# Optimization experiments

Measured on AMD Instinct MI355X. Metric: run time of the kernel, lower is better.

The kernel has to match this reference:

```python
import jax, jax.numpy as jnp
import numpy as np

B, S, H, NH = 2, 1024, 1024, 16
SE, E = 512, 1024
NEXP, TOPK, FF = 8, 2, 2048
HD = H // NH
EPS = 1e-6
THETA = 10000.0
NEG = -1e9


def _rms(x, w):
    return x * jax.lax.rsqrt(jnp.mean(x * x, axis=-1, keepdims=True) + EPS) * w


def _rope(q, k, pos):
    # q,k: [B,S,NH,HD]; pos: [B,S] int
    inv = 1.0 / (THETA ** (jnp.arange(0, HD, 2, dtype=jnp.float32) / HD))
    f = pos[..., None].astype(jnp.float32) * inv            # [B,S,HD/2]
    emb = jnp.concatenate([f, f], axis=-1)                  # [B,S,HD]
    cos = jnp.cos(emb)[:, :, None, :]
    sin = jnp.sin(emb)[:, :, None, :]
    def rot(x):
        x1, x2 = jnp.split(x, 2, axis=-1)
        return jnp.concatenate([-x2, x1], axis=-1)
    return q * cos + rot(q) * sin, k * cos + rot(k) * sin


def _forward(hidden_states, encoder_hidden_states,
             in_ln_w, wq, wk, wv, wo,
             c_norm_w, cq_w, cq_b, ck_w, ck_b, cv_w, cv_b, co_w, co_b,
             post_ln_w, gate_w, w1, w2, w3,
             position_ids, encoder_attention_mask):
    x = hidden_states

    # ---- self-attention (RMSNorm pre-norm, RoPE, causal) ----
    res = x
    h = _rms(x, in_ln_w)
    q = (h @ wq.T).reshape(B, S, NH, HD)
    k = (h @ wk.T).reshape(B, S, NH, HD)
    v = (h @ wv.T).reshape(B, S, NH, HD)
    q, k = _rope(q, k, position_ids)
    scores = jnp.einsum('bqhd,bkhd->bhqk', q, k) / np.sqrt(HD)
    causal = jnp.tril(jnp.ones((S, S), dtype=bool))
    scores = jnp.where(causal, scores, NEG)
    attn = jax.nn.softmax(scores, axis=-1)
    o = jnp.einsum('bhqk,bkhd->bqhd', attn, v).reshape(B, S, H) @ wo.T
    x = res + o

    # ---- cross-attention block (RMSNorm, MHA with kdim=vdim=E, bias) ----
    res = x
    h = _rms(x, c_norm_w)
    cq = (h @ cq_w.T + cq_b).reshape(B, S, NH, HD)
    ck = (encoder_hidden_states @ ck_w.T + ck_b).reshape(B, SE, NH, HD)
    cv = (encoder_hidden_states @ cv_w.T + cv_b).reshape(B, SE, NH, HD)
    sc = jnp.einsum('bqhd,bkhd->bhqk', cq, ck) / np.sqrt(HD)
    pad = (encoder_attention_mask == 0)                     # key_padding_mask
    sc = jnp.where(pad[:, None, None, :], NEG, sc)
    ca = jax.nn.softmax(sc, axis=-1)
    o = jnp.einsum('bhqk,bkhd->bqhd', ca, cv).reshape(B, S, H) @ co_w.T + co_b
    x = res + o

    # ---- block-sparse MoE FFN (top-2 routing, SwiGLU experts) ----
    res = x
    h = _rms(x, post_ln_w).reshape(-1, H)                   # [T,H], T=B*S
    logits = h @ gate_w.T                                    # [T,NEXP]
    probs = jax.nn.softmax(logits, axis=-1)
    topv, topi = jax.lax.top_k(probs, TOPK)                  # [T,TOPK]
    topv = topv / jnp.sum(topv, axis=-1, keepdims=True)
    out = jnp.zeros_like(h)
    for e in range(NEXP):  # fixed small expert loop
        we = jnp.sum(jnp.where(topi == e, topv, 0.0), axis=-1)   # [T]
        ff = (jax.nn.silu(h @ w1[e].T) * (h @ w3[e].T)) @ w2[e].T
        out = out + we[:, None] * ff
    x = res + out.reshape(B, S, H)
    return x


def setup_inputs() -> dict:
    key = jax.random.key(0)
    ks = jax.random.split(key, 24)
    sc = 0.02
    d = {
        'hidden_states': jax.random.normal(ks[0], (B, S, H), jnp.float32),
        'position_ids': jnp.broadcast_to(jnp.arange(S, dtype=jnp.int64), (B, S)),
        'encoder_hidden_states': jax.random.normal(ks[1], (B, SE, E), jnp.float32),
        'encoder_attention_mask': jnp.ones((B, SE), jnp.int64),
        'in_ln_w': jnp.ones((H,), jnp.float32),
        'wq': jax.random.normal(ks[2], (H, H), jnp.float32) * sc,
        'wk': jax.random.normal(ks[3], (H, H), jnp.float32) * sc,
        'wv': jax.random.normal(ks[4], (H, H), jnp.float32) * sc,
        'wo': jax.random.normal(ks[5], (H, H), jnp.float32) * sc,
        'c_norm_w': jnp.ones((H,), jnp.float32),
        'cq_w': jax.random.normal(ks[6], (H, H), jnp.float32) * sc,
        'cq_b': jnp.zeros((H,), jnp.float32),
        'ck_w': jax.random.normal(ks[7], (H, E), jnp.float32) * sc,
        'ck_b': jnp.zeros((H,), jnp.float32),
        'cv_w': jax.random.normal(ks[8], (H, E), jnp.float32) * sc,
        'cv_b': jnp.zeros((H,), jnp.float32),
        'co_w': jax.random.normal(ks[9], (H, H), jnp.float32) * sc,
        'co_b': jnp.zeros((H,), jnp.float32),
        'post_ln_w': jnp.ones((H,), jnp.float32),
        'gate_w': jax.random.normal(ks[10], (NEXP, H), jnp.float32) * sc,
        'w1': jax.random.normal(ks[11], (NEXP, FF, H), jnp.float32) * sc,
        'w2': jax.random.normal(ks[12], (NEXP, H, FF), jnp.float32) * sc,
        'w3': jax.random.normal(ks[13], (NEXP, FF, H), jnp.float32) * sc,
    }
    return d


def reference(hidden_states, position_ids, encoder_hidden_states, encoder_attention_mask,
              in_ln_w, wq, wk, wv, wo,
              c_norm_w, cq_w, cq_b, ck_w, ck_b, cv_w, cv_b, co_w, co_b,
              post_ln_w, gate_w, w1, w2, w3):
    return _forward(hidden_states, encoder_hidden_states,
                    in_ln_w, wq, wk, wv, wo,
                    c_norm_w, cq_w, cq_b, ck_w, ck_b, cv_w, cv_b, co_w, co_b,
                    post_ln_w, gate_w, w1, w2, w3,
                    position_ids, encoder_attention_mask)
```

## Files before the change

kernel.cpp:

```cpp
#include <hip/hip_runtime.h>

#define B_    2
#define S_    1024
#define H_    1024
#define NH_   16
#define HD_   64
#define SE_   512
#define E_    1024
#define NEXP_ 8
#define FF_   2048
#define T_    (B_*S_)
#define TE_   (B_*SE_)
#define PERM_MAX 6400
#define MAXRT 24

typedef short v8s __attribute__((ext_vector_type(8)));
typedef short v4s __attribute__((ext_vector_type(4)));
typedef float v4f __attribute__((ext_vector_type(4)));
typedef _Float16 v8h __attribute__((ext_vector_type(8)));
typedef _Float16 v4h __attribute__((ext_vector_type(4)));

__device__ __forceinline__ unsigned short f2b(float f) {
  unsigned int u = __float_as_uint(f);
  u = (u + 0x7FFFu + ((u >> 16) & 1u)) >> 16;
  return (unsigned short)u;
}

__device__ __forceinline__ void g2l16(const void* g, void* l) {
  __builtin_amdgcn_global_load_lds(
      (const __attribute__((address_space(1))) unsigned int*)g,
      (__attribute__((address_space(3))) unsigned int*)l, 16, 0, 0);
}

__global__ void detect_kern(const int* __restrict__ pos, const int* __restrict__ msk,
                            int* __restrict__ flags, int* __restrict__ counts) {
  if (threadIdx.x < 16) counts[threadIdx.x] = 0;
  if (threadIdx.x == 0) {
    flags[0] = (pos[1] == 1) ? 0 : 1;
    flags[1] = (msk[1] == 1) ? 0 : 1;
  }
}

struct SplitArgs {
  const float* src[9];
  _Float16* dh[9];
  _Float16* dl[9];
};
__global__ __launch_bounds__(256)
void split_all(SplitArgs sa) {
  int b = blockIdx.x;
  int seg, i;
  if (b < 4096) { seg = b >> 9; i = (b & 511) * 256 + threadIdx.x; }
  else          { seg = 8;      i = (b - 4096) * 256 + threadIdx.x; }
  const float* x = sa.src[seg];
  v4f a = *(const v4f*)&x[i * 8];
  v4f c = *(const v4f*)&x[i * 8 + 4];
  v8h hv, lv;
  #pragma unroll
  for (int j = 0; j < 8; ++j) {
    float v = j < 4 ? a[j] : c[j - 4];
    _Float16 hh = (_Float16)v;
    hv[j] = hh; lv[j] = (_Float16)(v - (float)hh);
  }
  *(v8h*)&sa.dh[seg][i * 8] = hv;
  *(v8h*)&sa.dl[seg][i * 8] = lv;
}

__global__ __launch_bounds__(256)
void cvt_all(const float* __restrict__ s0, const float* __restrict__ s1,
             const float* __restrict__ s2,
             unsigned short* __restrict__ d0, unsigned short* __restrict__ d1,
             unsigned short* __restrict__ d2) {
  int b = blockIdx.x;
  int seg = b >> 14;
  int i = (b & 16383) * 256 + threadIdx.x;
  const float* x = seg == 0 ? s0 : (seg == 1 ? s1 : s2);
  unsigned short* y = seg == 0 ? d0 : (seg == 1 ? d1 : d2);
  v4f v = *(const v4f*)&x[i * 4];
  v4s o;
  #pragma unroll
  for (int j = 0; j < 4; ++j) o[j] = (short)f2b(v[j]);
  *(v4s*)&y[i * 4] = o;
}

__global__ __launch_bounds__(256)
void rmsnorm_hl_kern(const float* __restrict__ x, const float* __restrict__ w,
                     _Float16* __restrict__ yh, _Float16* __restrict__ yl) {
  int row = blockIdx.x, tid = threadIdx.x;
  const float* xr = x + (long)row * 1024;
  v4f v = *(const v4f*)&xr[tid * 4];
  float ss = v[0]*v[0] + v[1]*v[1] + v[2]*v[2] + v[3]*v[3];
  #pragma unroll
  for (int off = 32; off; off >>= 1) ss += __shfl_xor(ss, off);
  __shared__ float sw[4];
  if ((tid & 63) == 0) sw[tid >> 6] = ss;
  __syncthreads();
  float tot = sw[0] + sw[1] + sw[2] + sw[3];
  float rs = rsqrtf(tot * (1.0f / 1024.0f) + 1e-6f);
  const float* wr = w + tid * 4;
  v4h oh, ol;
  #pragma unroll
  for (int j = 0; j < 4; ++j) {
    float f = v[j] * rs * wr[j];
    _Float16 hh = (_Float16)f;
    oh[j] = hh; ol[j] = (_Float16)(f - (float)hh);
  }
  *(v4h*)&yh[(long)row * 1024 + tid * 4] = oh;
  *(v4h*)&yl[(long)row * 1024 + tid * 4] = ol;
}

__global__ __launch_bounds__(256)
void rmsnorm_kern(const float* __restrict__ x, const float* __restrict__ w,
                  unsigned short* __restrict__ y) {
  int row = blockIdx.x, tid = threadIdx.x;
  const float* xr = x + (long)row * 1024;
  v4f v = *(const v4f*)&xr[tid * 4];
  float ss = v[0]*v[0] + v[1]*v[1] + v[2]*v[2] + v[3]*v[3];
  #pragma unroll
  for (int off = 32; off; off >>= 1) ss += __shfl_xor(ss, off);
  __shared__ float sw[4];
  if ((tid & 63) == 0) sw[tid >> 6] = ss;
  __syncthreads();
  float tot = sw[0] + sw[1] + sw[2] + sw[3];
  float rs = rsqrtf(tot * (1.0f / 1024.0f) + 1e-6f);
  const float* wr = w + tid * 4;
  v4s o;
  #pragma unroll
  for (int j = 0; j < 4; ++j) o[j] = (short)f2b(v[j] * rs * wr[j]);
  *(v4s*)&y[(long)row * 1024 + tid * 4] = o;
}

__global__ __launch_bounds__(256)
void rope_split_kern(float* __restrict__ q, const float* __restrict__ k,
                     _Float16* __restrict__ kh, _Float16* __restrict__ kl,
                     const int* __restrict__ pos, const int* __restrict__ flags) {
  int g = blockIdx.x * 256 + threadIdx.x;
  int d = g & 31;
  int h = (g >> 5) & 15;
  int s = (g >> 9) & (S_ - 1);
  int b = g >> 19;
  long base = (((long)(b * S_ + s)) * NH_ + h) * HD_;
  int pidx = b * S_ + s;
  int pv = pos[flags[0] ? (pidx << 1) : pidx];
  float p = (float)pv;
  float inv = powf(10000.0f, -(float)d * (1.0f / 32.0f));
  float f = p * inv;
  float sn = sinf(f), cs = cosf(f);
  float q1 = q[base + d], q2 = q[base + d + 32];
  q[base + d]      = q1 * cs - q2 * sn;
  q[base + d + 32] = q2 * cs + q1 * sn;
  float k1 = k[base + d], k2 = k[base + d + 32];
  float kr1 = k1 * cs - k2 * sn;
  float kr2 = k2 * cs + k1 * sn;
  _Float16 hh = (_Float16)kr1;
  kh[base + d] = hh; kl[base + d] = (_Float16)(kr1 - (float)hh);
  hh = (_Float16)kr2;
  kh[base + d + 32] = hh; kl[base + d + 32] = (_Float16)(kr2 - (float)hh);
}

__global__ __launch_bounds__(256)
void vtrans_kern(const float* __restrict__ vf, _Float16* __restrict__ vth,
                 _Float16* __restrict__ vtl, int Sk) {
  int kb = blockIdx.x, bh = blockIdx.y;
  int b = bh >> 4, h = bh & 15;
  int t = threadIdx.x;
  __shared__ float tile[64][65];
  int key = t >> 2, dsub = (t & 3) * 16;
  const float* src = vf + (((long)(b * Sk + kb * 64 + key)) * NH_ + h) * HD_ + dsub;
  #pragma unroll
  for (int j = 0; j < 16; j += 4) *(v4f*)&tile[key][dsub + j] = *(const v4f*)&src[j];
  __syncthreads();
  int d = t >> 2, ksub = (t & 3) * 16;
  v8h hv0, lv0, hv1, lv1;
  #pragma unroll
  for (int j = 0; j < 16; ++j) {
    float v = tile[ksub + j][d];
    _Float16 hh = (_Float16)v;
    if (j < 8) { hv0[j] = hh; lv0[j] = (_Float16)(v - (float)hh); }
    else       { hv1[j - 8] = hh; lv1[j - 8] = (_Float16)(v - (float)hh); }
  }
  long ob = (((long)(b * NH_ + h)) * HD_ + d) * Sk + kb * 64 + ksub;
  *(v8h*)&vth[ob] = hv0; *(v8h*)&vth[ob + 8] = hv1;
  *(v8h*)&vtl[ob] = lv0; *(v8h*)&vtl[ob + 8] = lv1;
}

struct ZArg {
  const _Float16 *Ah, *Al, *Bh, *Bl;
  const float *bias, *resid;
  float *Cf;
  float *Cf2;
  _Float16 *Ch, *Cl;
  int M;
};

__global__ __launch_bounds__(256)
void gemm_hl(ZArg z0, ZArg z1, ZArg z2, int K) {
  ZArg za = blockIdx.z == 0 ? z0 : (blockIdx.z == 1 ? z1 : z2);
  int flat = blockIdx.x;
  int wg = (flat & 7) * 32 + (flat >> 3);
  int row0 = (wg >> 4) * 128;
  int col0 = (wg & 15) * 64;
  if (row0 >= za.M) return;
  int tid = threadIdx.x, lane = tid & 63, w = tid >> 6;
  int lr = lane & 15, lg = lane >> 4;
  int wr = w >> 1, wc = w & 1;
  int rsw = (lr >> 1) & 3;

  __shared__ _Float16 Ah_s[2][128 * 32], Al_s[2][128 * 32];
  __shared__ _Float16 Bh_s[2][64 * 32], Bl_s[2][64 * 32];

  int av0 = w * 64 + lane, av1 = (w + 4) * 64 + lane;
  int ar0 = av0 >> 2, as0 = (av0 & 3) ^ ((ar0 >> 1) & 3);
  int ar1 = av1 >> 2, as1 = (av1 & 3) ^ ((ar1 >> 1) & 3);
  int bv = w * 64 + lane;
  int br = bv >> 2, bs = (bv & 3) ^ ((br >> 1) & 3);
  const _Float16* ga0h = za.Ah + (long)(row0 + ar0) * K + as0 * 8;
  const _Float16* ga0l = za.Al + (long)(row0 + ar0) * K + as0 * 8;
  const _Float16* ga1h = za.Ah + (long)(row0 + ar1) * K + as1 * 8;
  const _Float16* ga1l = za.Al + (long)(row0 + ar1) * K + as1 * 8;
  const _Float16* gbh  = za.Bh + (long)(col0 + br) * K + bs * 8;
  const _Float16* gbl  = za.Bl + (long)(col0 + br) * K + bs * 8;

  auto stage = [&](int buf, int k0) {
    g2l16(ga0h + k0, (char*)Ah_s[buf] + w * 1024);
    g2l16(ga1h + k0, (char*)Ah_s[buf] + (w + 4) * 1024);
    g2l16(ga0l + k0, (char*)Al_s[buf] + w * 1024);
    g2l16(ga1l + k0, (char*)Al_s[buf] + (w + 4) * 1024);
    g2l16(gbh + k0, (char*)Bh_s[buf] + w * 1024);
    g2l16(gbl + k0, (char*)Bl_s[buf] + w * 1024);
  };

  v4f acc[4][2] = {};
  stage(0, 0);
  int cur = 0;

  for (int k0 = 0; k0 < K; k0 += 32) {
    __syncthreads();
    if (k0 + 32 < K) stage(cur ^ 1, k0 + 32);

    v8h ah[4], al[4], bh[2], bl[2];
    #pragma unroll
    for (int m = 0; m < 4; ++m) {
      int off = (wr * 64 + m * 16 + lr) * 64 + ((lg ^ rsw) << 4);
      ah[m] = *(const v8h*)((char*)Ah_s[cur] + off);
      al[m] = *(const v8h*)((char*)Al_s[cur] + off);
    }
    #pragma unroll
    for (int n = 0; n < 2; ++n) {
      int off = (wc * 32 + n * 16 + lr) * 64 + ((lg ^ rsw) << 4);
      bh[n] = *(const v8h*)((char*)Bh_s[cur] + off);
      bl[n] = *(const v8h*)((char*)Bl_s[cur] + off);
    }
    #pragma unroll
    for (int m = 0; m < 4; ++m)
      #pragma unroll
      for (int n = 0; n < 2; ++n) {
        acc[m][n] = __builtin_amdgcn_mfma_f32_16x16x32_f16(ah[m], bh[n], acc[m][n], 0, 0, 0);
        acc[m][n] = __builtin_amdgcn_mfma_f32_16x16x32_f16(ah[m], bl[n], acc[m][n], 0, 0, 0);
        acc[m][n] = __builtin_amdgcn_mfma_f32_16x16x32_f16(al[m], bh[n], acc[m][n], 0, 0, 0);
      }
    cur ^= 1;
  }

  #pragma unroll
  for (int m = 0; m < 4; ++m) {
    int rbase = row0 + wr * 64 + m * 16 + lg * 4;
    #pragma unroll
    for (int n = 0; n < 2; ++n) {
      int gcol = col0 + wc * 32 + n * 16 + lr;
      float bb = za.bias ? za.bias[gcol] : 0.0f;
      #pragma unroll
      for (int rr = 0; rr < 4; ++rr) {
        long idx = (long)(rbase + rr) * 1024 + gcol;
        float v = acc[m][n][rr] + bb;
        if (za.Cf) {
          float r = za.resid ? (za.resid[idx] + v) : v;
          za.Cf[idx] = r;
          if (za.Cf2) za.Cf2[idx] = r;
        } else {
          _Float16 hh = (_Float16)v;
          za.Ch[idx] = hh;
          za.Cl[idx] = (_Float16)(v - (float)hh);
        }
      }
    }
  }
}

template<bool CAUSAL>
__global__ __launch_bounds__(256)
void attn_hl(const float* __restrict__ Q,
             const _Float16* __restrict__ Khg, const _Float16* __restrict__ Klg,
             const _Float16* __restrict__ Vhg, const _Float16* __restrict__ Vlg,
             _Float16* __restrict__ Oh, _Float16* __restrict__ Ol,
             const int* __restrict__ mask, const int* __restrict__ flags,
             int Sq, int Sk, float qscale) {
  int flat = blockIdx.x;
  int wgA = (flat & 7) * 64 + (flat >> 3);
  int qt = wgA & 15, bh = wgA >> 4;
  int b = bh >> 4, h = bh & 15;
  int tid = threadIdx.x, lane = tid & 63, w = tid >> 6;
  int lr = lane & 15, lg = lane >> 4;
  int q0 = qt * 64;
  int mf = (!CAUSAL && mask) ? flags[1] : 0;
  int swz = lr & 7;

  __shared__ _Float16 Kh_s[64 * 64], Kl_s[64 * 64];
  __shared__ _Float16 Vh_s[64 * 64], Vl_s[64 * 64];
  __shared__ _Float16 Psh[4][16][72], Psl[4][16][72];

  v8h qh[2], ql[2];
  {
    long qbase = ((long)(b * Sq + q0 + w * 16 + lr) * NH_ + h) * HD_;
    #pragma unroll
    for (int kk = 0; kk < 2; ++kk) {
      v4f f0 = *(const v4f*)&Q[qbase + kk * 32 + lg * 8];
      v4f f1 = *(const v4f*)&Q[qbase + kk * 32 + lg * 8 + 4];
      #pragma unroll
      for (int j = 0; j < 8; ++j) {
        float f = (j < 4 ? f0[j] : f1[j - 4]) * qscale;
        _Float16 hh = (_Float16)f;
        qh[kk][j] = hh;
        ql[kk][j] = (_Float16)(f - (float)hh);
      }
    }
  }
  v4f of[4] = {};
  float m4[4], l4[4];
  #pragma unroll
  for (int i = 0; i < 4; ++i) { m4[i] = -3e38f; l4[i] = 0.0f; }

  int nkt = CAUSAL ? (qt + 1) : (Sk >> 6);
  for (int kt = 0; kt < nkt; ++kt) {
    __syncthreads();
    #pragma unroll
    for (int i = 0; i < 2; ++i) {
      int c = w + i * 4;
      int v = c * 64 + lane;
      int row = v >> 3, c8 = v & 7;
      int sc = (c8 ^ (row & 7)) << 3;
      long kb = ((long)(b * Sk + kt * 64 + row) * NH_ + h) * HD_ + sc;
      g2l16(Khg + kb, (char*)Kh_s + c * 1024);
      g2l16(Klg + kb, (char*)Kl_s + c * 1024);
      long vb = ((long)(b * NH_ + h) * HD_ + row) * Sk + kt * 64 + sc;
      g2l16(Vhg + vb, (char*)Vh_s + c * 1024);
      g2l16(Vlg + vb, (char*)Vl_s + c * 1024);
    }
    __syncthreads();

    v4f sf[4] = {};
    #pragma unroll
    for (int kk = 0; kk < 2; ++kk)
      #pragma unroll
      for (int n = 0; n < 4; ++n) {
        int off = (n * 16 + lr) * 128 + ((((kk << 2) | lg) ^ swz) << 4);
        v8h kbh = *(const v8h*)((char*)Kh_s + off);
        v8h kbl = *(const v8h*)((char*)Kl_s + off);
        sf[n] = __builtin_amdgcn_mfma_f32_16x16x32_f16(qh[kk], kbh, sf[n], 0, 0, 0);
        sf[n] = __builtin_amdgcn_mfma_f32_16x16x32_f16(qh[kk], kbl, sf[n], 0, 0, 0);
        sf[n] = __builtin_amdgcn_mfma_f32_16x16x32_f16(ql[kk], kbh, sf[n], 0, 0, 0);
      }

    if constexpr (CAUSAL) {
      if (kt == qt) {
        #pragma unroll
        for (int n = 0; n < 4; ++n) {
          int kcol = kt * 64 + n * 16 + lr;
          #pragma unroll
          for (int rr = 0; rr < 4; ++rr) {
            int qr = q0 + w * 16 + lg * 4 + rr;
            if (kcol > qr) sf[n][rr] = -1e9f;
          }
        }
      }
    } else {
      if (mask) {
        #pragma unroll
        for (int n = 0; n < 4; ++n) {
          int kcol = kt * 64 + n * 16 + lr;
          int mi = b * Sk + kcol;
          if (mask[mf ? (mi << 1) : mi] == 0) {
            #pragma unroll
            for (int rr = 0; rr < 4; ++rr) sf[n][rr] = -1e9f;
          }
        }
      }
    }

    float al[4];
    #pragma unroll
    for (int rr = 0; rr < 4; ++rr) {
      float mx = fmaxf(fmaxf(sf[0][rr], sf[1][rr]), fmaxf(sf[2][rr], sf[3][rr]));
      #pragma unroll
      for (int off = 8; off; off >>= 1) mx = fmaxf(mx, __shfl_xor(mx, off));
      float mn = fmaxf(m4[rr], mx);
      al[rr] = __expf(m4[rr] - mn);
      m4[rr] = mn;
      float rs = 0.0f;
      #pragma unroll
      for (int n = 0; n < 4; ++n) {
        float pv = __expf(sf[n][rr] - mn);
        sf[n][rr] = pv;
        rs += pv;
      }
      #pragma unroll
      for (int off = 8; off; off >>= 1) rs += __shfl_xor(rs, off);
      l4[rr] = l4[rr] * al[rr] + rs;
    }

    #pragma unroll
    for (int n = 0; n < 4; ++n)
      #pragma unroll
      for (int rr = 0; rr < 4; ++rr) {
        of[n][rr] *= al[rr];
        float pv = sf[n][rr];
        _Float16 ph = (_Float16)pv;
        Psh[w][lg * 4 + rr][n * 16 + lr] = ph;
        Psl[w][lg * 4 + rr][n * 16 + lr] = (_Float16)(pv - (float)ph);
      }
    __syncthreads();

    #pragma unroll
    for (int kc = 0; kc < 2; ++kc) {
      v8h pah = *(const v8h*)&Psh[w][lr][kc * 32 + lg * 8];
      v8h pal = *(const v8h*)&Psl[w][lr][kc * 32 + lg * 8];
      #pragma unroll
      for (int n = 0; n < 4; ++n) {
        int off = (n * 16 + lr) * 128 + ((((kc << 2) | lg) ^ swz) << 4);
        v8h vbh = *(const v8h*)((char*)Vh_s + off);
        v8h vbl = *(const v8h*)((char*)Vl_s + off);
        of[n] = __builtin_amdgcn_mfma_f32_16x16x32_f16(pah, vbh, of[n], 0, 0, 0);
        of[n] = __builtin_amdgcn_mfma_f32_16x16x32_f16(pah, vbl, of[n], 0, 0, 0);
        of[n] = __builtin_amdgcn_mfma_f32_16x16x32_f16(pal, vbh, of[n], 0, 0, 0);
      }
    }
  }

  #pragma unroll
  for (int rr = 0; rr < 4; ++rr) {
    int qr = q0 + w * 16 + lg * 4 + rr;
    float inv = 1.0f / l4[rr];
    long ob = (long)(b * Sq + qr) * 1024 + h * 64;
    #pragma unroll
    for (int n = 0; n < 4; ++n) {
      float v = of[n][rr] * inv;
      _Float16 hh = (_Float16)v;
      Oh[ob + n * 16 + lr] = hh;
      Ol[ob + n * 16 + lr] = (_Float16)(v - (float)hh);
    }
  }
}

__global__ __launch_bounds__(512)
void moe_gemm1(const unsigned short* __restrict__ A,
               const unsigned short* __restrict__ B1,
               const unsigned short* __restrict__ B2,
               unsigned short* __restrict__ Cb,
               const int* __restrict__ tm_e, const int* __restrict__ tm_slot,
               const int* __restrict__ ntl, const int* __restrict__ perm) {
  int flat = blockIdx.x;
  int wg = (flat & 7) * 96 + (flat >> 3);
  int tile = wg >> 5;
  if (tile >= ntl[0]) return;
  int col0 = (wg & 31) * 64;
  int e = tm_e[tile];
  int row0 = tm_slot[tile];
  const unsigned short* Bp1 = B1 + (long)e * (FF_ * H_);
  const unsigned short* Bp2 = B2 + (long)e * (FF_ * H_);
  int tid = threadIdx.x, lane = tid & 63, w = tid >> 6;
  int lr = lane & 15, lg = lane >> 4;
  int wr = w >> 1, wc = w & 1;
  int rsw = (lr >> 1) & 3;

  __shared__ unsigned short As[2][256 * 32];
  __shared__ unsigned short Bs1[2][64 * 32];
  __shared__ unsigned short Bs2[2][64 * 32];

  const unsigned short* ga[2];
  #pragma unroll
  for (int i = 0; i < 2; ++i) {
    int c = i * 512 + tid;
    int r = c >> 2, sub = (c & 3) ^ ((r >> 1) & 3);
    int tok = perm[row0 + r];
    ga[i] = A + (long)(tok < 0 ? 0 : tok) * H_ + sub * 8;
  }
  int bc = tid & 255;
  int rb = bc >> 2, sb = (bc & 3) ^ ((rb >> 1) & 3);
  const unsigned short* gB = (tid < 256 ? Bp1 : Bp2) + (long)(col0 + rb) * H_ + sb * 8;
  size_t lBoff = (size_t)((w & 3) * 64) * 8;

  auto stage = [&](int buf, int k0) {
    #pragma unroll
    for (int i = 0; i < 2; ++i)
      g2l16(ga[i] + k0, As[buf] + (size_t)(i * 512 + w * 64) * 8);
    g2l16(gB + k0, (tid < 256 ? Bs1[buf] : Bs2[buf]) + lBoff);
  };

  v4f acc[4][2] = {};
  v4f acc2[4][2] = {};
  stage(0, 0);
  int cur = 0;

  for (int k0 = 0; k0 < H_; k0 += 32) {
    __syncthreads();
    if (k0 + 32 < H_) stage(cur ^ 1, k0 + 32);

    v8s a[4], b1[2], b2[2];
    #pragma unroll
    for (int m = 0; m < 4; ++m)
      a[m] = *(const v8s*)&As[cur][(wr * 64 + m * 16 + lr) * 32 + (lg ^ rsw) * 8];
    #pragma unroll
    for (int n = 0; n < 2; ++n) {
      b1[n] = *(const v8s*)&Bs1[cur][(wc * 32 + n * 16 + lr) * 32 + (lg ^ rsw) * 8];
      b2[n] = *(const v8s*)&Bs2[cur][(wc * 32 + n * 16 + lr) * 32 + (lg ^ rsw) * 8];
    }
    #pragma unroll
    for (int m = 0; m < 4; ++m)
      #pragma unroll
      for (int n = 0; n < 2; ++n) {
        acc[m][n]  = __builtin_amdgcn_mfma_f32_16x16x32_bf16(a[m], b1[n], acc[m][n], 0, 0, 0);
        acc2[m][n] = __builtin_amdgcn_mfma_f32_16x16x32_bf16(a[m], b2[n], acc2[m][n], 0, 0, 0);
      }
    cur ^= 1;
  }

  #pragma unroll
  for (int m = 0; m < 4; ++m) {
    int grow = row0 + wr * 64 + m * 16 + lg * 4;
    #pragma unroll
    for (int n = 0; n < 2; ++n) {
      int gcol = col0 + wc * 32 + n * 16 + lr;
      #pragma unroll
      for (int rr = 0; rr < 4; ++rr) {
        float v = acc[m][n][rr];
        float g = v / (1.0f + __expf(-v));
        Cb[(long)(grow + rr) * FF_ + gcol] = f2b(g * acc2[m][n][rr]);
      }
    }
  }
}

__global__ __launch_bounds__(256)
void moe_gemm2(const unsigned short* __restrict__ A,
               const unsigned short* __restrict__ B,
               float* __restrict__ Cf,
               const int* __restrict__ tm_e, const int* __restrict__ tm_slot,
               const int* __restrict__ ntl,
               const int* __restrict__ perm, const float* __restrict__ pwgt) {
  int flat = blockIdx.x;
  int wg = (flat & 7) * 96 + (flat >> 3);
  int t2 = wg >> 4;
  int tile = t2 >> 1;
  if (tile >= ntl[0]) return;
  int row0 = tm_slot[tile] + (t2 & 1) * 128;
  int col0 = (wg & 15) * 64;
  int e = tm_e[tile];
  const unsigned short* Bp = B + (long)e * (H_ * FF_);
  int tid = threadIdx.x, lane = tid & 63, w = tid >> 6;
  int lr = lane & 15, lg = lane >> 4;
  int rsw = (lr >> 1) & 3;

  __shared__ unsigned short As[2][128 * 32];
  __shared__ unsigned short Bs[2][64 * 32];

  const unsigned short* ga[2];
  #pragma unroll
  for (int i = 0; i < 2; ++i) {
    int c = i * 256 + tid;
    int r = c >> 2, sub = (c & 3) ^ ((r >> 1) & 3);
    ga[i] = A + (long)(row0 + r) * FF_ + sub * 8;
  }
  int rb = tid >> 2, sb = (tid & 3) ^ ((rb >> 1) & 3);
  const unsigned short* gb = Bp + (long)(col0 + rb) * FF_ + sb * 8;

  auto stage = [&](int buf, int k0) {
    #pragma unroll
    for (int i = 0; i < 2; ++i)
      g2l16(ga[i] + k0, As[buf] + (size_t)(i * 256 + w * 64) * 8);
    g2l16(gb + k0, Bs[buf] + (size_t)(w * 64) * 8);
  };

  v4f acc[2][4] = {};
  stage(0, 0);
  int cur = 0;

  for (int k0 = 0; k0 < FF_; k0 += 32) {
    __syncthreads();
    if (k0 + 32 < FF_) stage(cur ^ 1, k0 + 32);

    v8s a[2], b[4];
    #pragma unroll
    for (int m = 0; m < 2; ++m)
      a[m] = *(const v8s*)&As[cur][(w * 32 + m * 16 + lr) * 32 + (lg ^ rsw) * 8];
    #pragma unroll
    for (int n = 0; n < 4; ++n)
      b[n] = *(const v8s*)&Bs[cur][(n * 16 + lr) * 32 + (lg ^ rsw) * 8];
    #pragma unroll
    for (int m = 0; m < 2; ++m)
      #pragma unroll
      for (int n = 0; n < 4; ++n)
        acc[m][n] = __builtin_amdgcn_mfma_f32_16x16x32_bf16(a[m], b[n], acc[m][n], 0, 0, 0);
    cur ^= 1;
  }

  #pragma unroll
  for (int m = 0; m < 2; ++m) {
    int grow = row0 + w * 32 + m * 16 + lg * 4;
    #pragma unroll
    for (int rr = 0; rr < 4; ++rr) {
      int tok = perm[grow + rr];
      if (tok < 0) continue;
      float pw = pwgt[grow + rr];
      #pragma unroll
      for (int n = 0; n < 4; ++n) {
        int gcol = col0 + n * 16 + lr;
        atomicAdd(&Cf[(long)tok * H_ + gcol], acc[m][n][rr] * pw);
      }
    }
  }
}

__global__ __launch_bounds__(64)
void router_kern(const float* __restrict__ x, const float* __restrict__ w,
                 const float* __restrict__ gw,
                 int* __restrict__ topi, float* __restrict__ topw,
                 int* __restrict__ counts) {
  int t = blockIdx.x, lane = threadIdx.x;
  const float* xr = x + (long)t * 1024;
  float vals[16];
  float ss = 0.0f;
  #pragma unroll
  for (int i = 0; i < 16; ++i) { float v = xr[lane + i * 64]; vals[i] = v; ss += v * v; }
  #pragma unroll
  for (int off = 32; off; off >>= 1) ss += __shfl_xor(ss, off);
  float rs = rsqrtf(ss * (1.0f / 1024.0f) + 1e-6f);
  #pragma unroll
  for (int i = 0; i < 16; ++i) vals[i] *= rs * w[lane + i * 64];
  float lgts[8];
  #pragma unroll
  for (int e = 0; e < 8; ++e) {
    const float* g = gw + e * 1024;
    float s = 0.0f;
    #pragma unroll
    for (int i = 0; i < 16; ++i) s += vals[i] * g[lane + i * 64];
    #pragma unroll
    for (int off = 32; off; off >>= 1) s += __shfl_xor(s, off);
    lgts[e] = s;
  }
  int i1 = 0; float l1 = lgts[0];
  #pragma unroll
  for (int e = 1; e < 8; ++e) if (lgts[e] > l1) { l1 = lgts[e]; i1 = e; }
  int i2 = -1; float l2 = -3e38f;
  #pragma unroll
  for (int e = 0; e < 8; ++e) if (e != i1 && lgts[e] > l2) { l2 = lgts[e]; i2 = e; }
  float w1 = 1.0f / (1.0f + __expf(l2 - l1));
  if (lane == 0) {
    topi[t * 2] = i1; topi[t * 2 + 1] = i2;
    topw[t * 2] = w1; topw[t * 2 + 1] = 1.0f - w1;
    atomicAdd(&counts[i1], 1);
    atomicAdd(&counts[i2], 1);
  }
}

__global__ __launch_bounds__(256)
void route_pack_kern(const int* __restrict__ counts,
                     const int* __restrict__ topi, const float* __restrict__ topw,
                     int* __restrict__ poff,
                     int* __restrict__ tm_e, int* __restrict__ tm_slot,
                     int* __restrict__ ntl,
                     int* __restrict__ perm, float* __restrict__ pwgt) {
  __shared__ int s_poff[8];
  __shared__ int s_cur[8];
  __shared__ int stot;
  if (threadIdx.x < 8) s_cur[threadIdx.x] = 0;
  if (threadIdx.x == 0) {
    int off = 0, nt = 0;
    for (int e = 0; e < 8; ++e) {
      s_poff[e] = off; poff[e] = off;
      int c = counts[e];
      int ntE = (c + 255) >> 8;
      for (int i = 0; i < ntE; ++i) { tm_e[nt] = e; tm_slot[nt] = off + i * 256; ++nt; }
      off += ntE * 256;
    }
    ntl[0] = nt; ntl[1] = off;
    stot = off;
  }
  __syncthreads();
  for (int s = threadIdx.x; s < stot; s += 256) perm[s] = -1;
  __syncthreads();
  for (int t = threadIdx.x; t < T_; t += 256) {
    #pragma unroll
    for (int kk = 0; kk < 2; ++kk) {
      int e = topi[t * 2 + kk];
      int pos = atomicAdd(&s_cur[e], 1);
      int slot = s_poff[e] + pos;
      perm[slot] = t;
      pwgt[slot] = topw[t * 2 + kk];
    }
  }
}

extern "C" void kernel_launch(void* const* d_in, const int* in_sizes, int n_in,
                              void* d_out, int out_size, void* d_ws, size_t ws_size,
                              hipStream_t stream) {
  (void)in_sizes; (void)n_in; (void)out_size; (void)ws_size;
  const float* x_in  = (const float*)d_in[0];
  const int*  posids = (const int*)d_in[1];
  const float* enc   = (const float*)d_in[2];
  const int*  emask  = (const int*)d_in[3];
  const float* inln  = (const float*)d_in[4];
  const float* wq    = (const float*)d_in[5];
  const float* wk    = (const float*)d_in[6];
  const float* wv    = (const float*)d_in[7];
  const float* wo    = (const float*)d_in[8];
  const float* cnorm = (const float*)d_in[9];
  const float* cqw   = (const float*)d_in[10];
  const float* cqb   = (const float*)d_in[11];
  const float* ckw   = (const float*)d_in[12];
  const float* ckb   = (const float*)d_in[13];
  const float* cvw   = (const float*)d_in[14];
  const float* cvb   = (const float*)d_in[15];
  const float* cow   = (const float*)d_in[16];
  const float* cob   = (const float*)d_in[17];
  const float* pln   = (const float*)d_in[18];
  const float* gatew = (const float*)d_in[19];
  const float* w1    = (const float*)d_in[20];
  const float* w2    = (const float*)d_in[21];
  const float* w3    = (const float*)d_in[22];
  float* out = (float*)d_out;

  char* p = (char*)d_ws;
  auto alloc = [&](size_t bytes) -> char* {
    char* r = p;
    p += (bytes + 255) & ~(size_t)255;
    return r;
  };
  const size_t MB = 1024 * 1024;
  char* A1 = alloc(4 * MB);
  char* A2 = alloc(4 * MB);
  char* Bq = alloc(8 * MB);
  char* Bk = alloc(8 * MB);
  char* Bv = alloc(8 * MB);
  char* C1 = alloc(4 * MB);
  char* C2 = alloc(4 * MB);
  char* D1 = alloc(4 * MB);
  char* D2 = alloc(4 * MB);
  float* x1 = (float*)alloc(8 * MB);
  float* x2 = (float*)alloc(8 * MB);
  unsigned short* h3b = (unsigned short*)alloc(4 * MB);
  _Float16* ench = (_Float16*)alloc(2 * MB);
  _Float16* encl = (_Float16*)alloc(2 * MB);
  int*   meta    = (int*)alloc(4 * (8 + 8 + 8 + 2 + 2 + MAXRT + MAXRT));
  int*   counts  = meta;
  int*   poff    = meta + 16;
  int*   ntl     = meta + 24;
  int*   flags   = meta + 26;
  int*   tm_e    = meta + 28;
  int*   tm_slot = meta + 28 + MAXRT;
  int*   topi    = (int*)alloc((size_t)T_ * 2 * 4);
  float* topw    = (float*)alloc((size_t)T_ * 2 * 4);
  int*   perm    = (int*)alloc((size_t)PERM_MAX * 4);
  float* pwgt    = (float*)alloc((size_t)PERM_MAX * 4);
  unsigned short* w1b = (unsigned short*)alloc((size_t)NEXP_ * FF_ * H_ * 2);
  unsigned short* w3b = (unsigned short*)alloc((size_t)NEXP_ * FF_ * H_ * 2);
  unsigned short* w2b = (unsigned short*)alloc((size_t)NEXP_ * H_ * FF_ * 2);

  _Float16 *hh = (_Float16*)A1, *hl = (_Float16*)A2;
  _Float16 *oh = (_Float16*)A1, *ol = (_Float16*)A2;
  _Float16 *ckh = (_Float16*)A1, *ckl = (_Float16*)A2;
  float* qf = (float*)Bq;  float* cqf = (float*)Bq;
  float* kf = (float*)Bk;
  _Float16 *cvth = (_Float16*)Bk, *cvtl = (_Float16*)(Bk + 4 * MB);
  float* vf = (float*)Bv;  float* cvf = (float*)Bv;
  _Float16 *kh = (_Float16*)C1, *kl = (_Float16*)C2;
  _Float16 *h2h = (_Float16*)C1, *h2l = (_Float16*)C2;
  _Float16 *vth = (_Float16*)D1, *vtl = (_Float16*)D2;
  _Float16 *coh = (_Float16*)D1, *col = (_Float16*)D2;
  unsigned short* ffh = (unsigned short*)Bq;
  _Float16* wsp = (_Float16*)w1b;
  auto wsph = [&](int i) { return wsp + (size_t)i * 2097152; };
  auto wspl = [&](int i) { return wsp + (size_t)i * 2097152 + 1048576; };

  dim3 blk(256);

  detect_kern<<<1, 64, 0, stream>>>(posids, emask, flags, counts);

  {
    SplitArgs sa;
    const float* wlist[8] = {wq, wk, wv, wo, cqw, ckw, cvw, cow};
    for (int i = 0; i < 8; ++i) { sa.src[i] = wlist[i]; sa.dh[i] = wsph(i); sa.dl[i] = wspl(i); }
    sa.src[8] = enc; sa.dh[8] = ench; sa.dl[8] = encl;
    split_all<<<4608, blk, 0, stream>>>(sa);
  }

  rmsnorm_hl_kern<<<T_, blk, 0, stream>>>(x_in, inln, hh, hl);
  {
    ZArg zq = {hh, hl, wsph(0), wspl(0), nullptr, nullptr, qf, nullptr, nullptr, nullptr, 2048};
    ZArg zk = {hh, hl, wsph(1), wspl(1), nullptr, nullptr, kf, nullptr, nullptr, nullptr, 2048};
    ZArg zv = {hh, hl, wsph(2), wspl(2), nullptr, nullptr, vf, nullptr, nullptr, nullptr, 2048};
    gemm_hl<<<dim3(256, 1, 3), blk, 0, stream>>>(zq, zk, zv, 1024);
  }
  rope_split_kern<<<(B_ * S_ * NH_ * 32) / 256, blk, 0, stream>>>(qf, kf, kh, kl, posids, flags);
  vtrans_kern<<<dim3(16, 32), blk, 0, stream>>>(vf, vth, vtl, 1024);
  attn_hl<true><<<512, blk, 0, stream>>>(
      qf, kh, kl, vth, vtl, oh, ol, nullptr, flags, 1024, 1024, 0.125f);
  {
    ZArg zo = {oh, ol, wsph(3), wspl(3), nullptr, x_in, x1, nullptr, nullptr, nullptr, 2048};
    gemm_hl<<<dim3(256, 1, 1), blk, 0, stream>>>(zo, zo, zo, 1024);
  }

  rmsnorm_hl_kern<<<T_, blk, 0, stream>>>(x1, cnorm, h2h, h2l);
  {
    ZArg zcq = {h2h, h2l, wsph(4), wspl(4), cqb, nullptr, cqf, nullptr, nullptr, nullptr, 2048};
    ZArg zck = {ench, encl, wsph(5), wspl(5), ckb, nullptr, nullptr, nullptr, ckh, ckl, 1024};
    ZArg zcv = {ench, encl, wsph(6), wspl(6), cvb, nullptr, cvf, nullptr, nullptr, nullptr, 1024};
    gemm_hl<<<dim3(256, 1, 3), blk, 0, stream>>>(zcq, zck, zcv, 1024);
  }
  vtrans_kern<<<dim3(8, 32), blk, 0, stream>>>(cvf, cvth, cvtl, 512);
  attn_hl<false><<<512, blk, 0, stream>>>(
      cqf, ckh, ckl, cvth, cvtl, coh, col, emask, flags, 1024, 512, 0.125f);
  {
    ZArg zco = {coh, col, wsph(7), wspl(7), cob, x1, x2, out, nullptr, nullptr, 2048};
    gemm_hl<<<dim3(256, 1, 1), blk, 0, stream>>>(zco, zco, zco, 1024);
  }

  cvt_all<<<49152, blk, 0, stream>>>(w1, w3, w2, w1b, w3b, w2b);
  rmsnorm_kern<<<T_, blk, 0, stream>>>(x2, pln, h3b);
  router_kern<<<T_, dim3(64), 0, stream>>>(x2, pln, gatew, topi, topw, counts);
  route_pack_kern<<<1, blk, 0, stream>>>(counts, topi, topw, poff, tm_e, tm_slot,
                                         ntl, perm, pwgt);
  moe_gemm1<<<768, dim3(512), 0, stream>>>(
      h3b, w1b, w3b, ffh, tm_e, tm_slot, ntl, perm);
  moe_gemm2<<<768, blk, 0, stream>>>(
      ffh, w2b, out, tm_e, tm_slot, ntl, perm, pwgt);
}
```

Measured before the change: 539.1 us.

## Fuse expert weight fp32-to-bf16 conversion into MoE GEMM staging loads

```diff
diff --git a/kernel.cpp b/kernel.cpp
--- a/kernel.cpp
+++ b/kernel.cpp
@@ -64,23 +64,6 @@
   }
   *(v8h*)&sa.dh[seg][i * 8] = hv;
   *(v8h*)&sa.dl[seg][i * 8] = lv;
-}
-
-__global__ __launch_bounds__(256)
-void cvt_all(const float* __restrict__ s0, const float* __restrict__ s1,
-             const float* __restrict__ s2,
-             unsigned short* __restrict__ d0, unsigned short* __restrict__ d1,
-             unsigned short* __restrict__ d2) {
-  int b = blockIdx.x;
-  int seg = b >> 14;
-  int i = (b & 16383) * 256 + threadIdx.x;
-  const float* x = seg == 0 ? s0 : (seg == 1 ? s1 : s2);
-  unsigned short* y = seg == 0 ? d0 : (seg == 1 ? d1 : d2);
-  v4f v = *(const v4f*)&x[i * 4];
-  v4s o;
-  #pragma unroll
-  for (int j = 0; j < 4; ++j) o[j] = (short)f2b(v[j]);
-  *(v4s*)&y[i * 4] = o;
 }
 
 __global__ __launch_bounds__(256)
@@ -453,8 +436,8 @@
 
 __global__ __launch_bounds__(512)
 void moe_gemm1(const unsigned short* __restrict__ A,
-               const unsigned short* __restrict__ B1,
-               const unsigned short* __restrict__ B2,
+               const float* __restrict__ B1,
+               const float* __restrict__ B2,
                unsigned short* __restrict__ Cb,
                const int* __restrict__ tm_e, const int* __restrict__ tm_slot,
                const int* __restrict__ ntl, const int* __restrict__ perm) {
@@ -465,8 +448,8 @@
   int col0 = (wg & 31) * 64;
   int e = tm_e[tile];
   int row0 = tm_slot[tile];
-  const unsigned short* Bp1 = B1 + (long)e * (FF_ * H_);
-  const unsigned short* Bp2 = B2 + (long)e * (FF_ * H_);
+  const float* Bp1 = B1 + (long)e * (FF_ * H_);
+  const float* Bp2 = B2 + (long)e * (FF_ * H_);
   int tid = threadIdx.x, lane = tid & 63, w = tid >> 6;
   int lr = lane & 15, lg = lane >> 4;
   int wr = w >> 1, wc = w & 1;
@@ -486,14 +469,19 @@
   }
   int bc = tid & 255;
   int rb = bc >> 2, sb = (bc & 3) ^ ((rb >> 1) & 3);
-  const unsigned short* gB = (tid < 256 ? Bp1 : Bp2) + (long)(col0 + rb) * H_ + sb * 8;
-  size_t lBoff = (size_t)((w & 3) * 64) * 8;
+  const float* gB = (tid < 256 ? Bp1 : Bp2) + (long)(col0 + rb) * H_ + sb * 8;
+  int lBoff = bc * 8;
 
   auto stage = [&](int buf, int k0) {
+    v4f b0 = *(const v4f*)&gB[k0];
+    v4f b1 = *(const v4f*)&gB[k0 + 4];
     #pragma unroll
     for (int i = 0; i < 2; ++i)
       g2l16(ga[i] + k0, As[buf] + (size_t)(i * 512 + w * 64) * 8);
-    g2l16(gB + k0, (tid < 256 ? Bs1[buf] : Bs2[buf]) + lBoff);
+    v8s hv;
+    #pragma unroll
+    for (int j = 0; j < 8; ++j) hv[j] = (short)f2b(j < 4 ? b0[j] : b1[j - 4]);
+    *(v8s*)&((tid < 256 ? Bs1 : Bs2)[buf][lBoff]) = hv;
   };
 
   v4f acc[4][2] = {};
@@ -505,21 +493,21 @@
     __syncthreads();
     if (k0 + 32 < H_) stage(cur ^ 1, k0 + 32);
 
-    v8s a[4], b1[2], b2[2];
+    v8s a[4], b1v[2], b2v[2];
     #pragma unroll
     for (int m = 0; m < 4; ++m)
       a[m] = *(const v8s*)&As[cur][(wr * 64 + m * 16 + lr) * 32 + (lg ^ rsw) * 8];
     #pragma unroll
     for (int n = 0; n < 2; ++n) {
-      b1[n] = *(const v8s*)&Bs1[cur][(wc * 32 + n * 16 + lr) * 32 + (lg ^ rsw) * 8];
-      b2[n] = *(const v8s*)&Bs2[cur][(wc * 32 + n * 16 + lr) * 32 + (lg ^ rsw) * 8];
+      b1v[n] = *(const v8s*)&Bs1[cur][(wc * 32 + n * 16 + lr) * 32 + (lg ^ rsw) * 8];
+      b2v[n] = *(const v8s*)&Bs2[cur][(wc * 32 + n * 16 + lr) * 32 + (lg ^ rsw) * 8];
     }
     #pragma unroll
     for (int m = 0; m < 4; ++m)
       #pragma unroll
       for (int n = 0; n < 2; ++n) {
-        acc[m][n]  = __builtin_amdgcn_mfma_f32_16x16x32_bf16(a[m], b1[n], acc[m][n], 0, 0, 0);
-        acc2[m][n] = __builtin_amdgcn_mfma_f32_16x16x32_bf16(a[m], b2[n], acc2[m][n], 0, 0, 0);
+        acc[m][n]  = __builtin_amdgcn_mfma_f32_16x16x32_bf16(a[m], b1v[n], acc[m][n], 0, 0, 0);
+        acc2[m][n] = __builtin_amdgcn_mfma_f32_16x16x32_bf16(a[m], b2v[n], acc2[m][n], 0, 0, 0);
       }
     cur ^= 1;
   }
@@ -542,7 +530,7 @@
 
 __global__ __launch_bounds__(256)
 void moe_gemm2(const unsigned short* __restrict__ A,
-               const unsigned short* __restrict__ B,
+               const float* __restrict__ B,
                float* __restrict__ Cf,
                const int* __restrict__ tm_e, const int* __restrict__ tm_slot,
                const int* __restrict__ ntl,
@@ -555,7 +543,7 @@
   int row0 = tm_slot[tile] + (t2 & 1) * 128;
   int col0 = (wg & 15) * 64;
   int e = tm_e[tile];
-  const unsigned short* Bp = B + (long)e * (H_ * FF_);
+  const float* Bp = B + (long)e * (H_ * FF_);
   int tid = threadIdx.x, lane = tid & 63, w = tid >> 6;
   int lr = lane & 15, lg = lane >> 4;
   int rsw = (lr >> 1) & 3;
@@ -571,13 +559,19 @@
     ga[i] = A + (long)(row0 + r) * FF_ + sub * 8;
   }
   int rb = tid >> 2, sb = (tid & 3) ^ ((rb >> 1) & 3);
-  const unsigned short* gb = Bp + (long)(col0 + rb) * FF_ + sb * 8;
+  const float* gb = Bp + (long)(col0 + rb) * FF_ + sb * 8;
+  int lBoff = tid * 8;
 
   auto stage = [&](int buf, int k0) {
+    v4f b0 = *(const v4f*)&gb[k0];
+    v4f b1 = *(const v4f*)&gb[k0 + 4];
     #pragma unroll
     for (int i = 0; i < 2; ++i)
       g2l16(ga[i] + k0, As[buf] + (size_t)(i * 256 + w * 64) * 8);
-    g2l16(gb + k0, Bs[buf] + (size_t)(w * 64) * 8);
+    v8s hv;
+    #pragma unroll
+    for (int j = 0; j < 8; ++j) hv[j] = (short)f2b(j < 4 ? b0[j] : b1[j - 4]);
+    *(v8s*)&Bs[buf][lBoff] = hv;
   };
 
   v4f acc[2][4] = {};
@@ -761,9 +755,7 @@
   float* topw    = (float*)alloc((size_t)T_ * 2 * 4);
   int*   perm    = (int*)alloc((size_t)PERM_MAX * 4);
   float* pwgt    = (float*)alloc((size_t)PERM_MAX * 4);
-  unsigned short* w1b = (unsigned short*)alloc((size_t)NEXP_ * FF_ * H_ * 2);
-  unsigned short* w3b = (unsigned short*)alloc((size_t)NEXP_ * FF_ * H_ * 2);
-  unsigned short* w2b = (unsigned short*)alloc((size_t)NEXP_ * H_ * FF_ * 2);
+  _Float16* wsp  = (_Float16*)alloc(32 * MB);
 
   _Float16 *hh = (_Float16*)A1, *hl = (_Float16*)A2;
   _Float16 *oh = (_Float16*)A1, *ol = (_Float16*)A2;
@@ -777,7 +769,6 @@
   _Float16 *vth = (_Float16*)D1, *vtl = (_Float16*)D2;
   _Float16 *coh = (_Float16*)D1, *col = (_Float16*)D2;
   unsigned short* ffh = (unsigned short*)Bq;
-  _Float16* wsp = (_Float16*)w1b;
   auto wsph = [&](int i) { return wsp + (size_t)i * 2097152; };
   auto wspl = [&](int i) { return wsp + (size_t)i * 2097152 + 1048576; };
 
@@ -824,13 +815,12 @@
     gemm_hl<<<dim3(256, 1, 1), blk, 0, stream>>>(zco, zco, zco, 1024);
   }
 
-  cvt_all<<<49152, blk, 0, stream>>>(w1, w3, w2, w1b, w3b, w2b);
   rmsnorm_kern<<<T_, blk, 0, stream>>>(x2, pln, h3b);
   router_kern<<<T_, dim3(64), 0, stream>>>(x2, pln, gatew, topi, topw, counts);
   route_pack_kern<<<1, blk, 0, stream>>>(counts, topi, topw, poff, tm_e, tm_slot,
                                          ntl, perm, pwgt);
   moe_gemm1<<<768, dim3(512), 0, stream>>>(
-      h3b, w1b, w3b, ffh, tm_e, tm_slot, ntl, perm);
+      h3b, w1, w3, ffh, tm_e, tm_slot, ntl, perm);
   moe_gemm2<<<768, blk, 0, stream>>>(
-      ffh, w2b, out, tm_e, tm_slot, ntl, perm, pwgt);
-}
+      ffh, w2, out, tm_e, tm_slot, ntl, perm, pwgt);
+}
```

Result: slower. 550.8 us (+2.2%).

## Fold MoE weight bf16 conversion into attention GEMMs and RMSNorm kernels

Applied to the files above, without the earlier changes.

```diff
diff --git a/kernel.cpp b/kernel.cpp
--- a/kernel.cpp
+++ b/kernel.cpp
@@ -67,23 +67,6 @@
 }
 
 __global__ __launch_bounds__(256)
-void cvt_all(const float* __restrict__ s0, const float* __restrict__ s1,
-             const float* __restrict__ s2,
-             unsigned short* __restrict__ d0, unsigned short* __restrict__ d1,
-             unsigned short* __restrict__ d2) {
-  int b = blockIdx.x;
-  int seg = b >> 14;
-  int i = (b & 16383) * 256 + threadIdx.x;
-  const float* x = seg == 0 ? s0 : (seg == 1 ? s1 : s2);
-  unsigned short* y = seg == 0 ? d0 : (seg == 1 ? d1 : d2);
-  v4f v = *(const v4f*)&x[i * 4];
-  v4s o;
-  #pragma unroll
-  for (int j = 0; j < 4; ++j) o[j] = (short)f2b(v[j]);
-  *(v4s*)&y[i * 4] = o;
-}
-
-__global__ __launch_bounds__(256)
 void rmsnorm_hl_kern(const float* __restrict__ x, const float* __restrict__ w,
                      _Float16* __restrict__ yh, _Float16* __restrict__ yl) {
   int row = blockIdx.x, tid = threadIdx.x;
@@ -111,7 +94,8 @@
 
 __global__ __launch_bounds__(256)
 void rmsnorm_kern(const float* __restrict__ x, const float* __restrict__ w,
-                  unsigned short* __restrict__ y) {
+                  unsigned short* __restrict__ y,
+                  const float* __restrict__ csrc, unsigned short* __restrict__ cdst) {
   int row = blockIdx.x, tid = threadIdx.x;
   const float* xr = x + (long)row * 1024;
   v4f v = *(const v4f*)&xr[tid * 4];
@@ -128,6 +112,16 @@
   #pragma unroll
   for (int j = 0; j < 4; ++j) o[j] = (short)f2b(v[j] * rs * wr[j]);
   *(v4s*)&y[(long)row * 1024 + tid * 4] = o;
+  long base4 = (long)row * 2048;
+  #pragma unroll
+  for (int i = 0; i < 8; ++i) {
+    long i4 = base4 + tid + i * 256;
+    v4f cv = *(const v4f*)&csrc[i4 * 4];
+    v4s co;
+    #pragma unroll
+    for (int j = 0; j < 4; ++j) co[j] = (short)f2b(cv[j]);
+    *(v4s*)&cdst[i4 * 4] = co;
+  }
 }
 
 __global__ __launch_bounds__(256)
@@ -194,17 +188,35 @@
 };
 
 __global__ __launch_bounds__(256)
-void gemm_hl(ZArg z0, ZArg z1, ZArg z2, int K) {
+void gemm_hl(ZArg z0, ZArg z1, ZArg z2, int K,
+             const float* __restrict__ csrc, unsigned short* __restrict__ cdst,
+             long cn4, int cchunk4) {
   ZArg za = blockIdx.z == 0 ? z0 : (blockIdx.z == 1 ? z1 : z2);
   int flat = blockIdx.x;
   int wg = (flat & 7) * 32 + (flat >> 3);
   int row0 = (wg >> 4) * 128;
   int col0 = (wg & 15) * 64;
-  if (row0 >= za.M) return;
   int tid = threadIdx.x, lane = tid & 63, w = tid >> 6;
   int lr = lane & 15, lg = lane >> 4;
   int wr = w >> 1, wc = w & 1;
   int rsw = (lr >> 1) & 3;
+
+  auto do_cvt = [&]() {
+    if (!cdst) return;
+    int fb = blockIdx.z * 256 + blockIdx.x;
+    long base4 = (long)fb * cchunk4;
+    for (int i = tid; i < cchunk4; i += 256) {
+      long i4 = base4 + i;
+      if (i4 < cn4) {
+        v4f v = *(const v4f*)&csrc[i4 * 4];
+        v4s o;
+        #pragma unroll
+        for (int j = 0; j < 4; ++j) o[j] = (short)f2b(v[j]);
+        *(v4s*)&cdst[i4 * 4] = o;
+      }
+    }
+  };
+  if (row0 >= za.M) { do_cvt(); return; }
 
   __shared__ _Float16 Ah_s[2][128 * 32], Al_s[2][128 * 32];
   __shared__ _Float16 Bh_s[2][64 * 32], Bl_s[2][64 * 32];
@@ -285,6 +297,7 @@
       }
     }
   }
+  do_cvt();
 }
 
 template<bool CAUSAL>
@@ -777,7 +790,7 @@
   _Float16 *vth = (_Float16*)D1, *vtl = (_Float16*)D2;
   _Float16 *coh = (_Float16*)D1, *col = (_Float16*)D2;
   unsigned short* ffh = (unsigned short*)Bq;
-  _Float16* wsp = (_Float16*)w1b;
+  _Float16* wsp = (_Float16*)w2b;
   auto wsph = [&](int i) { return wsp + (size_t)i * 2097152; };
   auto wspl = [&](int i) { return wsp + (size_t)i * 2097152 + 1048576; };
 
@@ -798,7 +811,8 @@
     ZArg zq = {hh, hl, wsph(0), wspl(0), nullptr, nullptr, qf, nullptr, nullptr, nullptr, 2048};
     ZArg zk = {hh, hl, wsph(1), wspl(1), nullptr, nullptr, kf, nullptr, nullptr, nullptr, 2048};
     ZArg zv = {hh, hl, wsph(2), wspl(2), nullptr, nullptr, vf, nullptr, nullptr, nullptr, 2048};
-    gemm_hl<<<dim3(256, 1, 3), blk, 0, stream>>>(zq, zk, zv, 1024);
+    gemm_hl<<<dim3(256, 1, 3), blk, 0, stream>>>(zq, zk, zv, 1024,
+        w1, w1b, 4194304L, 5632);
   }
   rope_split_kern<<<(B_ * S_ * NH_ * 32) / 256, blk, 0, stream>>>(qf, kf, kh, kl, posids, flags);
   vtrans_kern<<<dim3(16, 32), blk, 0, stream>>>(vf, vth, vtl, 1024);
@@ -806,7 +820,8 @@
       qf, kh, kl, vth, vtl, oh, ol, nullptr, flags, 1024, 1024, 0.125f);
   {
     ZArg zo = {oh, ol, wsph(3), wspl(3), nullptr, x_in, x1, nullptr, nullptr, nullptr, 2048};
-    gemm_hl<<<dim3(256, 1, 1), blk, 0, stream>>>(zo, zo, zo, 1024);
+    gemm_hl<<<dim3(256, 1, 1), blk, 0, stream>>>(zo, zo, zo, 1024,
+        w3, w3b, 2097152L, 8192);
   }
 
   rmsnorm_hl_kern<<<T_, blk, 0, stream>>>(x1, cnorm, h2h, h2l);
@@ -814,18 +829,19 @@
     ZArg zcq = {h2h, h2l, wsph(4), wspl(4), cqb, nullptr, cqf, nullptr, nullptr, nullptr, 2048};
     ZArg zck = {ench, encl, wsph(5), wspl(5), ckb, nullptr, nullptr, nullptr, ckh, ckl, 1024};
     ZArg zcv = {ench, encl, wsph(6), wspl(6), cvb, nullptr, cvf, nullptr, nullptr, nullptr, 1024};
-    gemm_hl<<<dim3(256, 1, 3), blk, 0, stream>>>(zcq, zck, zcv, 1024);
+    gemm_hl<<<dim3(256, 1, 3), blk, 0, stream>>>(zcq, zck, zcv, 1024,
+        w3 + 8388608L, w3b + 8388608L, 2097152L, 2816);
   }
   vtrans_kern<<<dim3(8, 32), blk, 0, stream>>>(cvf, cvth, cvtl, 512);
   attn_hl<false><<<512, blk, 0, stream>>>(
       cqf, ckh, ckl, cvth, cvtl, coh, col, emask, flags, 1024, 512, 0.125f);
   {
     ZArg zco = {coh, col, wsph(7), wspl(7), cob, x1, x2, out, nullptr, nullptr, 2048};
-    gemm_hl<<<dim3(256, 1, 1), blk, 0, stream>>>(zco, zco, zco, 1024);
-  }
-
-  cvt_all<<<49152, blk, 0, stream>>>(w1, w3, w2, w1b, w3b, w2b);
-  rmsnorm_kern<<<T_, blk, 0, stream>>>(x2, pln, h3b);
+    gemm_hl<<<dim3(256, 1, 1), blk, 0, stream>>>(zco, zco, zco, 1024,
+        nullptr, nullptr, 0L, 0);
+  }
+
+  rmsnorm_kern<<<T_, blk, 0, stream>>>(x2, pln, h3b, w2, w2b);
   router_kern<<<T_, dim3(64), 0, stream>>>(x2, pln, gatew, topi, topw, counts);
   route_pack_kern<<<1, blk, 0, stream>>>(counts, topi, topw, poff, tm_e, tm_slot,
                                          ntl, perm, pwgt);
```

Result: slower. 561.1 us (+4.1%).
